# Optimization experiments

Hardware: AMD Instinct MI355X
Metric: run time of the kernel (lower is better)

## Reference

```python
import jax, jax.numpy as jnp
import numpy as np

NEG_SLOPE = 0.2


def _segment_softmax(scores, seg, num_segments):
    # scores: [nnz, H]; segment-wise (scatter) softmax, matching torch_geometric.utils.softmax
    m = jax.ops.segment_max(scores, seg, num_segments=num_segments)
    m = jnp.where(jnp.isfinite(m), m, 0.0)  # empty segments
    e = jnp.exp(scores - m[seg])
    s = jax.ops.segment_sum(e, seg, num_segments=num_segments)
    return e / (s[seg] + 1e-16)


def _class_partition(key, nnz, heads):
    # random permutation split into 4 class groups + inverse-permutation gather index
    perm = jax.random.permutation(key, nnz).astype(jnp.int32)
    q = nnz // 4
    parts = (perm[:q], perm[q:2 * q], perm[2 * q:3 * q], perm[3 * q:])
    inv = jnp.zeros((nnz,), jnp.int32).at[perm].set(jnp.arange(nnz, dtype=jnp.int32))
    gather_idx = jnp.broadcast_to(inv[:, None], (nnz, heads))
    return parts, gather_idx


def setup_inputs() -> dict:
    key = jax.random.key(0)
    N, M, NNZ = 100000, 50000, 800000
    IN_C, H, C = 128, 8, 16
    ks = jax.random.split(key, 9)
    X = jax.random.normal(ks[0], (N, IN_C), jnp.float32)
    vertex = jax.random.randint(ks[1], (NNZ,), 0, N, dtype=jnp.int32)
    edges = jax.random.randint(ks[2], (NNZ,), 0, M, dtype=jnp.int32)
    W_w = jax.random.normal(ks[3], (IN_C, H * C), jnp.float32) / np.float32(np.sqrt(IN_C))
    W_b = jnp.zeros((H * C,), jnp.float32)
    stdv = np.float32(np.sqrt(6.0 / (H + C)))
    att_e = jax.random.uniform(ks[4], (1, H, C), jnp.float32, -stdv, stdv)
    att_v = jax.random.uniform(ks[5], (1, H, C), jnp.float32, -stdv, stdv)
    (E0, E1, E2, E3), E_idx = _class_partition(ks[6], NNZ, H)
    (V0, V1, V2, V3), V_idx = _class_partition(ks[7], NNZ, H)
    return dict(X=X, vertex=vertex, edges=edges, W_w=W_w, W_b=W_b,
                att_e=att_e, att_v=att_v,
                E_class_index_0=E0, E_class_index_1=E1, E_class_index_2=E2, E_class_index_3=E3,
                E_class_index=E_idx,
                V_class_index_0=V0, V_class_index_1=V1, V_class_index_2=V2, V_class_index_3=V3,
                V_class_index=V_idx, edge_num=M)


def _class_scores(Xg, att, idx0, idx1, idx2, idx3):
    # (index_select by class, dot with att, sum over channel) then concat -> [nnz, H]
    parts = [jnp.sum(Xg[i] * att, axis=-1) for i in (idx0, idx1, idx2, idx3)]
    return jnp.concatenate(parts, axis=0)


def reference(X, vertex, edges, W_w, W_b, att_e, att_v,
              E_class_index_0, E_class_index_1, E_class_index_2, E_class_index_3, E_class_index,
              V_class_index_0, V_class_index_1, V_class_index_2, V_class_index_3, V_class_index,
              edge_num):
    N = X.shape[0]
    H, C = att_e.shape[1], att_e.shape[2]
    X0 = X @ W_w + W_b                       # [N, H*C]
    Xn = X0.reshape(N, H, C)
    Xve = Xn[vertex]                          # [nnz, H, C] gather node feats per incidence

    # vertex -> edge attention (edge-type-classed scores, segment softmax over hyperedges)
    Xe_cat = _class_scores(Xve, att_e, E_class_index_0, E_class_index_1, E_class_index_2, E_class_index_3)
    beta = jnp.take_along_axis(Xe_cat, E_class_index, axis=0)   # restore incidence order
    beta = jax.nn.leaky_relu(beta, NEG_SLOPE)
    beta = _segment_softmax(beta, edges, edge_num)              # [nnz, H]
    Xe = jax.ops.segment_sum(Xve * beta[..., None], edges, num_segments=edge_num)  # [M, H, C]
    Xe = jax.nn.relu(Xe)[edges]                                  # gather back: [nnz, H, C]

    # edge -> vertex attention (node-type-classed scores, segment softmax over vertices)
    Xa_cat = _class_scores(Xe, att_v, V_class_index_0, V_class_index_1, V_class_index_2, V_class_index_3)
    alpha = jnp.take_along_axis(Xa_cat, V_class_index, axis=0)
    alpha = jax.nn.leaky_relu(alpha, NEG_SLOPE)
    alpha = _segment_softmax(alpha, vertex, N)                   # [nnz, H]
    Xv = jax.ops.segment_sum(Xe * alpha[..., None], vertex, num_segments=N)  # [N, H, C]
    return Xv.reshape(N, H * C)
```

## Files before the change

kernel.cpp:

```cpp
#include <hip/hip_runtime.h>
#include <hip/hip_bf16.h>
#include <cstdint>
#include <cmath>

#define NEG_SLOPE 0.2f

static __device__ __forceinline__ float leaky(float x){ return x >= 0.f ? x : NEG_SLOPE*x; }

__global__ __launch_bounds__(256) void hist_rank_k(const int* __restrict__ edges, const int* __restrict__ vertex,
                                                   int* __restrict__ ce, int* __restrict__ cv,
                                                   int* __restrict__ re, int* __restrict__ rv, int nnz){
  int i = blockIdx.x*256 + threadIdx.x;
  if (i < nnz){
    re[i] = atomicAdd(&ce[edges[i]], 1);
    rv[i] = atomicAdd(&cv[vertex[i]], 1);
  }
}

__global__ __launch_bounds__(256) void scan_reduce_k(const int* __restrict__ ce, const int* __restrict__ cv,
                                                     int M, int N, int* __restrict__ partials){
  const int* src = blockIdx.y ? cv : ce;
  const int L = blockIdx.y ? N : M;
  const int base = blockIdx.x*2048;
  int s = 0;
  for (int j = threadIdx.x; j < 2048; j += 256){
    int idx = base + j;
    if (idx < L) s += src[idx];
  }
  for (int o = 32; o > 0; o >>= 1) s += __shfl_down(s, o);
  __shared__ int wsum[4];
  if ((threadIdx.x & 63) == 0) wsum[threadIdx.x >> 6] = s;
  __syncthreads();
  if (threadIdx.x == 0) partials[blockIdx.y*64 + blockIdx.x] = wsum[0]+wsum[1]+wsum[2]+wsum[3];
}

__global__ __launch_bounds__(128) void scan_partials_k(int* __restrict__ partials){
  const int w = threadIdx.x >> 6, l = threadIdx.x & 63;
  int v = partials[w*64 + l];
  int inc = v;
  for (int o = 1; o < 64; o <<= 1){ int u = __shfl_up(inc, o); if (l >= o) inc += u; }
  partials[w*64 + l] = inc - v;
}

__global__ __launch_bounds__(256) void scan_write_k(const int* __restrict__ ce, const int* __restrict__ cv,
                                                    int M, int N, const int* __restrict__ partials,
                                                    int* __restrict__ e_off, int* __restrict__ v_off){
  const int* src; int L; int* off;
  if (blockIdx.y == 0){ src = ce; L = M; off = e_off; }
  else                { src = cv; L = N; off = v_off; }
  const int base = blockIdx.x*2048 + threadIdx.x*8;
  int v[8];
  int tot = 0;
  #pragma unroll
  for (int j = 0; j < 8; ++j){ int idx = base+j; v[j] = (idx < L) ? src[idx] : 0; tot += v[j]; }
  const int lane = threadIdx.x & 63, wid = threadIdx.x >> 6;
  int inc = tot;
  for (int o = 1; o < 64; o <<= 1){ int u = __shfl_up(inc, o); if (lane >= o) inc += u; }
  __shared__ int wsum[4];
  if (lane == 63) wsum[wid] = inc;
  __syncthreads();
  int wbase = 0;
  for (int k = 0; k < wid; ++k) wbase += wsum[k];
  int run = partials[blockIdx.y*64 + blockIdx.x] + wbase + inc - tot;
  #pragma unroll
  for (int j = 0; j < 8; ++j){
    int idx = base + j;
    if (idx < L){
      off[idx] = run;
      run += v[j];
      if (idx == L-1) off[L] = run;
    }
  }
}

__global__ __launch_bounds__(256) void place_k(const int* __restrict__ edges, const int* __restrict__ vertex,
                                               const int* __restrict__ e_off, const int* __restrict__ v_off,
                                               const int* __restrict__ re, const int* __restrict__ rv,
                                               int* __restrict__ e_ent, int* __restrict__ v_ent, int nnz){
  int i = blockIdx.x*256 + threadIdx.x;
  if (i < nnz){
    atomicExch(&e_ent[e_off[edges[i]] + re[i]], i);
    atomicExch(&v_ent[v_off[vertex[i]] + rv[i]], i);
  }
}

__global__ __launch_bounds__(512) void gemm_k(const float* __restrict__ X, const float* __restrict__ W,
                                              const float* __restrict__ bias, const float* __restrict__ att_e,
                                              float* __restrict__ Y, float* __restrict__ sc_n, int N){
  __shared__ float Bs[64*128];
  __shared__ float As[64*65];
  __shared__ float att_s[128];
  const int t = threadIdx.x;
  if (t < 128) att_s[t] = att_e[t];
  const int row0 = blockIdx.x * 64;
  const int tr = t >> 4, tc = t & 15;
  const int r = tr*2;
  const int cA = tc*4, cB = 64 + tc*4;
  float acc[2][8];
  {
    float4 b0 = ((const float4*)bias)[tc];
    float4 b1 = ((const float4*)bias)[16 + tc];
    acc[0][0]=b0.x; acc[0][1]=b0.y; acc[0][2]=b0.z; acc[0][3]=b0.w;
    acc[0][4]=b1.x; acc[0][5]=b1.y; acc[0][6]=b1.z; acc[0][7]=b1.w;
    #pragma unroll
    for (int j = 0; j < 8; ++j) acc[1][j] = acc[0][j];
  }
  for (int kh = 0; kh < 2; ++kh){
    {
      const float4* W4 = (const float4*)(W + kh*64*128);
      float4* B4 = (float4*)Bs;
      #pragma unroll
      for (int j = 0; j < 4; ++j) B4[j*512 + t] = W4[j*512 + t];
      #pragma unroll
      for (int j = 0; j < 2; ++j){
        int idx = j*512 + t;
        int rr = idx >> 4, c4 = idx & 15;
        int gr = row0 + rr;
        float4 v = make_float4(0.f,0.f,0.f,0.f);
        if (gr < N) v = ((const float4*)X)[(size_t)gr*32 + kh*16 + c4];
        float* dst = &As[rr*65 + c4*4];
        dst[0]=v.x; dst[1]=v.y; dst[2]=v.z; dst[3]=v.w;
      }
    }
    __syncthreads();
    #pragma unroll 4
    for (int k = 0; k < 64; ++k){
      float a0 = As[r*65 + k], a1 = As[(r+1)*65 + k];
      const float4 w0 = *(const float4*)&Bs[k*128 + cA];
      const float4 w1 = *(const float4*)&Bs[k*128 + cB];
      float wv[8] = {w0.x,w0.y,w0.z,w0.w,w1.x,w1.y,w1.z,w1.w};
      #pragma unroll
      for (int j = 0; j < 8; ++j){ acc[0][j] += a0*wv[j]; acc[1][j] += a1*wv[j]; }
    }
    __syncthreads();
  }
  float pA0=0.f, pA1=0.f, pB0=0.f, pB1=0.f;
  #pragma unroll
  for (int j = 0; j < 4; ++j){
    float aa = att_s[cA + j], ab = att_s[cB + j];
    pA0 += acc[0][j]*aa;   pA1 += acc[1][j]*aa;
    pB0 += acc[0][4+j]*ab; pB1 += acc[1][4+j]*ab;
  }
  #pragma unroll
  for (int o = 1; o < 4; o <<= 1){
    pA0 += __shfl_xor(pA0, o); pA1 += __shfl_xor(pA1, o);
    pB0 += __shfl_xor(pB0, o); pB1 += __shfl_xor(pB1, o);
  }
  #pragma unroll
  for (int i = 0; i < 2; ++i){
    int gr = row0 + r + i;
    if (gr < N){
      float4 o0 = make_float4(acc[i][0],acc[i][1],acc[i][2],acc[i][3]);
      float4 o1 = make_float4(acc[i][4],acc[i][5],acc[i][6],acc[i][7]);
      float4* Y4 = (float4*)Y;
      Y4[(size_t)gr*32 + tc]      = o0;
      Y4[(size_t)gr*32 + 16 + tc] = o1;
    }
  }
  if ((tc & 3) == 0){
    int h = tc >> 2;
    int g0 = row0 + r, g1 = row0 + r + 1;
    if (g0 < N){ sc_n[(size_t)g0*8 + h] = leaky(pA0); sc_n[(size_t)g0*8 + 4 + h] = leaky(pB0); }
    if (g1 < N){ sc_n[(size_t)g1*8 + h] = leaky(pA1); sc_n[(size_t)g1*8 + 4 + h] = leaky(pB1); }
  }
}

template<bool STAGE1>
__global__ __launch_bounds__(256) void agg_k(const void* __restrict__ src_, const int* __restrict__ map,
                                             const float* __restrict__ sctab, const int* __restrict__ seg_off,
                                             const int* __restrict__ seg_ent, const float* __restrict__ att2,
                                             void* __restrict__ out_, float* __restrict__ sc_out, int nseg){
  __shared__ float s_lds[4][128][8];
  __shared__ int   r_lds[4][128];
  __shared__ float m_lds[4][8];
  __shared__ float d_lds[4][8];
  __shared__ float att_s[128];
  const float* srcf = (const float*)src_;
  const __hip_bfloat16* srcb = (const __hip_bfloat16*)src_;
  const int wid = threadIdx.x >> 6, lane = threadIdx.x & 63;
  if (STAGE1 && threadIdx.x < 128) att_s[threadIdx.x] = att2[threadIdx.x];
  const int seg = blockIdx.x*4 + wid;
  const bool active = seg < nseg;
  int start = 0, cnt = 0;
  if (active){ start = seg_off[seg]; cnt = seg_off[seg+1] - start; }
  const bool fits = (cnt <= 128);

  if (active && fits){
    for (int j = lane; j < cnt; j += 64){
      int id = seg_ent[start + j];
      int row = map[id];
      r_lds[wid][j] = row;
      const float4* sp = (const float4*)(sctab + (size_t)row*8);
      float4 x0 = sp[0], x1 = sp[1];
      float* dst = &s_lds[wid][j][0];
      ((float4*)dst)[0] = x0;
      ((float4*)dst)[1] = x1;
    }
  }
  __syncthreads();
  if (active && fits){
    const int h = lane & 7, jj = lane >> 3;
    float m = -INFINITY;
    for (int j = jj; j < cnt; j += 8) m = fmaxf(m, s_lds[wid][j][h]);
    #pragma unroll
    for (int o = 8; o < 64; o <<= 1) m = fmaxf(m, __shfl_xor(m, o));
    float s = 0.f;
    for (int j = jj; j < cnt; j += 8) s += __expf(s_lds[wid][j][h] - m);
    #pragma unroll
    for (int o = 8; o < 64; o <<= 1) s += __shfl_xor(s, o);
    if (lane < 8){ m_lds[wid][lane] = m; d_lds[wid][lane] = 1.f / (s + 1e-16f); }
  }
  __syncthreads();
  if (active && fits){
    for (int idx = lane; idx < cnt*8; idx += 64){
      int j = idx >> 3, h = idx & 7;
      s_lds[wid][j][h] = __expf(s_lds[wid][j][h] - m_lds[wid][h]) * d_lds[wid][h];
    }
  }
  __syncthreads();
  if (active){
    float acc0 = 0.f, acc1 = 0.f;
    const int ha = lane >> 4, hb = ha + 4;
    if (fits){
      for (int j = 0; j < cnt; ++j){
        float wa = s_lds[wid][j][ha];
        float wb = s_lds[wid][j][hb];
        float x0, x1;
        if (STAGE1){
          const float* xr = srcf + (size_t)r_lds[wid][j]*128;
          x0 = xr[lane]; x1 = xr[lane + 64];
        } else {
          const __hip_bfloat16* xr = srcb + (size_t)r_lds[wid][j]*128;
          x0 = __bfloat162float(xr[lane]); x1 = __bfloat162float(xr[lane + 64]);
        }
        acc0 += wa * x0;
        acc1 += wb * x1;
      }
    } else {
      float ma = -INFINITY, mb = -INFINITY;
      for (int j = 0; j < cnt; ++j){
        int id = seg_ent[start + j];
        int row = map[id];
        ma = fmaxf(ma, sctab[(size_t)row*8 + ha]);
        mb = fmaxf(mb, sctab[(size_t)row*8 + hb]);
      }
      float sa = 0.f, sb = 0.f;
      for (int j = 0; j < cnt; ++j){
        int id = seg_ent[start + j];
        int row = map[id];
        sa += __expf(sctab[(size_t)row*8 + ha] - ma);
        sb += __expf(sctab[(size_t)row*8 + hb] - mb);
      }
      float ra = 1.f/(sa + 1e-16f), rb = 1.f/(sb + 1e-16f);
      for (int j = 0; j < cnt; ++j){
        int id = seg_ent[start + j];
        int row = map[id];
        float wa = __expf(sctab[(size_t)row*8 + ha] - ma) * ra;
        float wb = __expf(sctab[(size_t)row*8 + hb] - mb) * rb;
        float x0, x1;
        if (STAGE1){
          const float* xr = srcf + (size_t)row*128;
          x0 = xr[lane]; x1 = xr[lane + 64];
        } else {
          const __hip_bfloat16* xr = srcb + (size_t)row*128;
          x0 = __bfloat162float(xr[lane]); x1 = __bfloat162float(xr[lane + 64]);
        }
        acc0 += wa * x0;
        acc1 += wb * x1;
      }
    }
    if (STAGE1){
      float o0 = fmaxf(acc0, 0.f);
      float o1 = fmaxf(acc1, 0.f);
      __hip_bfloat16* outb = (__hip_bfloat16*)out_;
      outb[(size_t)seg*128 + lane]      = __float2bfloat16(o0);
      outb[(size_t)seg*128 + 64 + lane] = __float2bfloat16(o1);
      float p0 = o0 * att_s[lane];
      float p1 = o1 * att_s[lane + 64];
      #pragma unroll
      for (int o = 1; o < 16; o <<= 1){ p0 += __shfl_xor(p0, o); p1 += __shfl_xor(p1, o); }
      if ((lane & 15) == 0){
        sc_out[(size_t)seg*8 + (lane >> 4)]     = leaky(p0);
        sc_out[(size_t)seg*8 + 4 + (lane >> 4)] = leaky(p1);
      }
    } else {
      float* outf = (float*)out_;
      outf[(size_t)seg*128 + lane]      = acc0;
      outf[(size_t)seg*128 + 64 + lane] = acc1;
    }
  }
}

extern "C" void kernel_launch(void* const* d_in, const int* in_sizes, int n_in,
                              void* d_out, int out_size, void* d_ws, size_t ws_size,
                              hipStream_t stream){
  const float* X      = (const float*)d_in[0];
  const int*   vertex = (const int*)d_in[1];
  const int*   edges  = (const int*)d_in[2];
  const float* W_w    = (const float*)d_in[3];
  const float* W_b    = (const float*)d_in[4];
  const float* att_e  = (const float*)d_in[5];
  const float* att_v  = (const float*)d_in[6];
  const int N   = in_sizes[0] / 128;
  const int NNZ = in_sizes[1];
  const int M   = 50000;

  char* p = (char*)d_ws;
  auto take = [&](size_t bytes)->void*{
    void* q = (void*)p;
    p += (bytes + 255) & ~(size_t)255;
    return q;
  };
  float* X0        = (float*)take((size_t)N*128*sizeof(float));
  __hip_bfloat16* Xe = (__hip_bfloat16*)take((size_t)M*128*sizeof(__hip_bfloat16));
  float* sc_n      = (float*)take((size_t)N*8*sizeof(float));
  float* sc_e      = (float*)take((size_t)M*8*sizeof(float));
  int*   e_off     = (int*)take((size_t)(M+1)*sizeof(int));
  int*   v_off     = (int*)take((size_t)(N+1)*sizeof(int));
  int*   e_cnt     = (int*)take((size_t)M*sizeof(int));
  int*   v_cnt     = (int*)take((size_t)N*sizeof(int));
  int*   re        = (int*)take((size_t)NNZ*sizeof(int));
  int*   rv        = (int*)take((size_t)NNZ*sizeof(int));
  int*   e_ent     = (int*)take((size_t)NNZ*sizeof(int));
  int*   v_ent     = (int*)take((size_t)NNZ*sizeof(int));
  int*   partials  = (int*)take(128*sizeof(int));

  hipMemsetAsync(e_cnt, 0, (size_t)M*sizeof(int), stream);
  hipMemsetAsync(v_cnt, 0, (size_t)N*sizeof(int), stream);

  gemm_k<<<dim3((N+63)/64), 512, 0, stream>>>(X, W_w, W_b, att_e, X0, sc_n, N);

  hist_rank_k<<<dim3((NNZ+255)/256), 256, 0, stream>>>(edges, vertex, e_cnt, v_cnt, re, rv, NNZ);
  const int LMAX = (N > M) ? N : M;
  const int nb = (LMAX + 2047)/2048;
  scan_reduce_k<<<dim3(nb,2), 256, 0, stream>>>(e_cnt, v_cnt, M, N, partials);
  scan_partials_k<<<dim3(1), 128, 0, stream>>>(partials);
  scan_write_k<<<dim3(nb,2), 256, 0, stream>>>(e_cnt, v_cnt, M, N, partials, e_off, v_off);
  place_k<<<dim3((NNZ+255)/256), 256, 0, stream>>>(edges, vertex, e_off, v_off, re, rv, e_ent, v_ent, NNZ);

  agg_k<true><<<dim3((M+3)/4), 256, 0, stream>>>(X0, vertex, sc_n, e_off, e_ent, att_v, Xe, sc_e, M);

  agg_k<false><<<dim3((N+3)/4), 256, 0, stream>>>(Xe, edges, sc_e, v_off, v_ent, nullptr, d_out, nullptr, N);
}
```

Before: 496.6 us.

## Store projected features in bf16 and put row ids directly in CSR entries

The projected node features X0 are now written in bf16 instead of fp32, which halves the bytes gathered in the first aggregation stage. The CSR placement now stores the neighbour row id directly rather than the incidence index, removing one level of indirect lookup per entry. Each lane now reads two adjacent channels with a single ushort2 load and handles one head, which simplifies the score reduction. The cost is lower precision in the intermediate features.

```diff
diff --git a/kernel.cpp b/kernel.cpp
--- a/kernel.cpp
+++ b/kernel.cpp
@@ -6,6 +6,14 @@
 #define NEG_SLOPE 0.2f
 
 static __device__ __forceinline__ float leaky(float x){ return x >= 0.f ? x : NEG_SLOPE*x; }
+static __device__ __forceinline__ unsigned short bf16bits(float x){
+  __hip_bfloat16 h = __float2bfloat16(x);
+  return *reinterpret_cast<unsigned short*>(&h);
+}
+static __device__ __forceinline__ float bfbits2f(unsigned short u){
+  unsigned v = ((unsigned)u) << 16;
+  return __uint_as_float(v);
+}
 
 __global__ __launch_bounds__(256) void hist_rank_k(const int* __restrict__ edges, const int* __restrict__ vertex,
                                                    int* __restrict__ ce, int* __restrict__ cv,
@@ -76,17 +84,18 @@
 __global__ __launch_bounds__(256) void place_k(const int* __restrict__ edges, const int* __restrict__ vertex,
                                                const int* __restrict__ e_off, const int* __restrict__ v_off,
                                                const int* __restrict__ re, const int* __restrict__ rv,
-                                               int* __restrict__ e_ent, int* __restrict__ v_ent, int nnz){
+                                               int* __restrict__ e_rows, int* __restrict__ v_rows, int nnz){
   int i = blockIdx.x*256 + threadIdx.x;
   if (i < nnz){
-    atomicExch(&e_ent[e_off[edges[i]] + re[i]], i);
-    atomicExch(&v_ent[v_off[vertex[i]] + rv[i]], i);
+    int e = edges[i], v = vertex[i];
+    atomicExch(&e_rows[e_off[e] + re[i]], v);
+    atomicExch(&v_rows[v_off[v] + rv[i]], e);
   }
 }
 
 __global__ __launch_bounds__(512) void gemm_k(const float* __restrict__ X, const float* __restrict__ W,
                                               const float* __restrict__ bias, const float* __restrict__ att_e,
-                                              float* __restrict__ Y, float* __restrict__ sc_n, int N){
+                                              __hip_bfloat16* __restrict__ Y, float* __restrict__ sc_n, int N){
   __shared__ float Bs[64*128];
   __shared__ float As[64*65];
   __shared__ float att_s[128];
@@ -150,11 +159,12 @@
   for (int i = 0; i < 2; ++i){
     int gr = row0 + r + i;
     if (gr < N){
-      float4 o0 = make_float4(acc[i][0],acc[i][1],acc[i][2],acc[i][3]);
-      float4 o1 = make_float4(acc[i][4],acc[i][5],acc[i][6],acc[i][7]);
-      float4* Y4 = (float4*)Y;
-      Y4[(size_t)gr*32 + tc]      = o0;
-      Y4[(size_t)gr*32 + 16 + tc] = o1;
+      ushort4 s0 = make_ushort4(bf16bits(acc[i][0]), bf16bits(acc[i][1]),
+                                bf16bits(acc[i][2]), bf16bits(acc[i][3]));
+      ushort4 s1 = make_ushort4(bf16bits(acc[i][4]), bf16bits(acc[i][5]),
+                                bf16bits(acc[i][6]), bf16bits(acc[i][7]));
+      *(ushort4*)((unsigned short*)Y + (size_t)gr*128 + cA) = s0;
+      *(ushort4*)((unsigned short*)Y + (size_t)gr*128 + cB) = s1;
     }
   }
   if ((tc & 3) == 0){
@@ -166,17 +176,16 @@
 }
 
 template<bool STAGE1>
-__global__ __launch_bounds__(256) void agg_k(const void* __restrict__ src_, const int* __restrict__ map,
+__global__ __launch_bounds__(256) void agg_k(const __hip_bfloat16* __restrict__ src,
                                              const float* __restrict__ sctab, const int* __restrict__ seg_off,
-                                             const int* __restrict__ seg_ent, const float* __restrict__ att2,
+                                             const int* __restrict__ seg_rows, const float* __restrict__ att2,
                                              void* __restrict__ out_, float* __restrict__ sc_out, int nseg){
   __shared__ float s_lds[4][128][8];
   __shared__ int   r_lds[4][128];
   __shared__ float m_lds[4][8];
   __shared__ float d_lds[4][8];
   __shared__ float att_s[128];
-  const float* srcf = (const float*)src_;
-  const __hip_bfloat16* srcb = (const __hip_bfloat16*)src_;
+  const unsigned short* srcu = (const unsigned short*)src;
   const int wid = threadIdx.x >> 6, lane = threadIdx.x & 63;
   if (STAGE1 && threadIdx.x < 128) att_s[threadIdx.x] = att2[threadIdx.x];
   const int seg = blockIdx.x*4 + wid;
@@ -187,8 +196,7 @@
 
   if (active && fits){
     for (int j = lane; j < cnt; j += 64){
-      int id = seg_ent[start + j];
-      int row = map[id];
+      int row = seg_rows[start + j];
       r_lds[wid][j] = row;
       const float4* sp = (const float4*)(sctab + (size_t)row*8);
       float4 x0 = sp[0], x1 = sp[1];
@@ -220,73 +228,45 @@
   __syncthreads();
   if (active){
     float acc0 = 0.f, acc1 = 0.f;
-    const int ha = lane >> 4, hb = ha + 4;
+    const int h2 = lane >> 3;
+    const int c2 = lane*2;
     if (fits){
       for (int j = 0; j < cnt; ++j){
-        float wa = s_lds[wid][j][ha];
-        float wb = s_lds[wid][j][hb];
-        float x0, x1;
-        if (STAGE1){
-          const float* xr = srcf + (size_t)r_lds[wid][j]*128;
-          x0 = xr[lane]; x1 = xr[lane + 64];
-        } else {
-          const __hip_bfloat16* xr = srcb + (size_t)r_lds[wid][j]*128;
-          x0 = __bfloat162float(xr[lane]); x1 = __bfloat162float(xr[lane + 64]);
-        }
-        acc0 += wa * x0;
-        acc1 += wb * x1;
+        float w = s_lds[wid][j][h2];
+        ushort2 u = *(const ushort2*)(srcu + (size_t)r_lds[wid][j]*128 + c2);
+        acc0 += w * bfbits2f(u.x);
+        acc1 += w * bfbits2f(u.y);
       }
     } else {
-      float ma = -INFINITY, mb = -INFINITY;
+      float m = -INFINITY;
       for (int j = 0; j < cnt; ++j){
-        int id = seg_ent[start + j];
-        int row = map[id];
-        ma = fmaxf(ma, sctab[(size_t)row*8 + ha]);
-        mb = fmaxf(mb, sctab[(size_t)row*8 + hb]);
-      }
-      float sa = 0.f, sb = 0.f;
+        int row = seg_rows[start + j];
+        m = fmaxf(m, sctab[(size_t)row*8 + h2]);
+      }
+      float s = 0.f;
       for (int j = 0; j < cnt; ++j){
-        int id = seg_ent[start + j];
-        int row = map[id];
-        sa += __expf(sctab[(size_t)row*8 + ha] - ma);
-        sb += __expf(sctab[(size_t)row*8 + hb] - mb);
-      }
-      float ra = 1.f/(sa + 1e-16f), rb = 1.f/(sb + 1e-16f);
+        int row = seg_rows[start + j];
+        s += __expf(sctab[(size_t)row*8 + h2] - m);
+      }
+      float rs = 1.f/(s + 1e-16f);
       for (int j = 0; j < cnt; ++j){
-        int id = seg_ent[start + j];
-        int row = map[id];
-        float wa = __expf(sctab[(size_t)row*8 + ha] - ma) * ra;
-        float wb = __expf(sctab[(size_t)row*8 + hb] - mb) * rb;
-        float x0, x1;
-        if (STAGE1){
-          const float* xr = srcf + (size_t)row*128;
-          x0 = xr[lane]; x1 = xr[lane + 64];
-        } else {
-          const __hip_bfloat16* xr = srcb + (size_t)row*128;
-          x0 = __bfloat162float(xr[lane]); x1 = __bfloat162float(xr[lane + 64]);
-        }
-        acc0 += wa * x0;
-        acc1 += wb * x1;
+        int row = seg_rows[start + j];
+        float w = __expf(sctab[(size_t)row*8 + h2] - m) * rs;
+        ushort2 u = *(const ushort2*)(srcu + (size_t)row*128 + c2);
+        acc0 += w * bfbits2f(u.x);
+        acc1 += w * bfbits2f(u.y);
       }
     }
     if (STAGE1){
       float o0 = fmaxf(acc0, 0.f);
       float o1 = fmaxf(acc1, 0.f);
-      __hip_bfloat16* outb = (__hip_bfloat16*)out_;
-      outb[(size_t)seg*128 + lane]      = __float2bfloat16(o0);
-      outb[(size_t)seg*128 + 64 + lane] = __float2bfloat16(o1);
-      float p0 = o0 * att_s[lane];
-      float p1 = o1 * att_s[lane + 64];
-      #pragma unroll
-      for (int o = 1; o < 16; o <<= 1){ p0 += __shfl_xor(p0, o); p1 += __shfl_xor(p1, o); }
-      if ((lane & 15) == 0){
-        sc_out[(size_t)seg*8 + (lane >> 4)]     = leaky(p0);
-        sc_out[(size_t)seg*8 + 4 + (lane >> 4)] = leaky(p1);
-      }
+      ushort2 uo = make_ushort2(bf16bits(o0), bf16bits(o1));
+      *(ushort2*)((unsigned short*)out_ + (size_t)seg*128 + c2) = uo;
+      float p = o0 * att_s[c2] + o1 * att_s[c2 + 1];
+      p += __shfl_xor(p, 1); p += __shfl_xor(p, 2); p += __shfl_xor(p, 4);
+      if ((lane & 7) == 0) sc_out[(size_t)seg*8 + h2] = leaky(p);
     } else {
-      float* outf = (float*)out_;
-      outf[(size_t)seg*128 + lane]      = acc0;
-      outf[(size_t)seg*128 + 64 + lane] = acc1;
+      *(float2*)((float*)out_ + (size_t)seg*128 + c2) = make_float2(acc0, acc1);
     }
   }
 }
@@ -311,7 +291,7 @@
     p += (bytes + 255) & ~(size_t)255;
     return q;
   };
-  float* X0        = (float*)take((size_t)N*128*sizeof(float));
+  __hip_bfloat16* X0 = (__hip_bfloat16*)take((size_t)N*128*sizeof(__hip_bfloat16));
   __hip_bfloat16* Xe = (__hip_bfloat16*)take((size_t)M*128*sizeof(__hip_bfloat16));
   float* sc_n      = (float*)take((size_t)N*8*sizeof(float));
   float* sc_e      = (float*)take((size_t)M*8*sizeof(float));
@@ -321,8 +301,8 @@
   int*   v_cnt     = (int*)take((size_t)N*sizeof(int));
   int*   re        = (int*)take((size_t)NNZ*sizeof(int));
   int*   rv        = (int*)take((size_t)NNZ*sizeof(int));
-  int*   e_ent     = (int*)take((size_t)NNZ*sizeof(int));
-  int*   v_ent     = (int*)take((size_t)NNZ*sizeof(int));
+  int*   e_rows    = (int*)take((size_t)NNZ*sizeof(int));
+  int*   v_rows    = (int*)take((size_t)NNZ*sizeof(int));
   int*   partials  = (int*)take(128*sizeof(int));
 
   hipMemsetAsync(e_cnt, 0, (size_t)M*sizeof(int), stream);
@@ -336,9 +316,9 @@
   scan_reduce_k<<<dim3(nb,2), 256, 0, stream>>>(e_cnt, v_cnt, M, N, partials);
   scan_partials_k<<<dim3(1), 128, 0, stream>>>(partials);
   scan_write_k<<<dim3(nb,2), 256, 0, stream>>>(e_cnt, v_cnt, M, N, partials, e_off, v_off);
-  place_k<<<dim3((NNZ+255)/256), 256, 0, stream>>>(edges, vertex, e_off, v_off, re, rv, e_ent, v_ent, NNZ);
-
-  agg_k<true><<<dim3((M+3)/4), 256, 0, stream>>>(X0, vertex, sc_n, e_off, e_ent, att_v, Xe, sc_e, M);
-
-  agg_k<false><<<dim3((N+3)/4), 256, 0, stream>>>(Xe, edges, sc_e, v_off, v_ent, nullptr, d_out, nullptr, N);
-}
+  place_k<<<dim3((NNZ+255)/256), 256, 0, stream>>>(edges, vertex, e_off, v_off, re, rv, e_rows, v_rows, NNZ);
+
+  agg_k<true><<<dim3((M+3)/4), 256, 0, stream>>>(X0, sc_n, e_off, e_rows, att_v, Xe, sc_e, M);
+
+  agg_k<false><<<dim3((N+3)/4), 256, 0, stream>>>(Xe, sc_e, v_off, v_rows, nullptr, d_out, nullptr, N);
+}
```

Result: faster. 454.7 us (-8.4%).
